# Kernel optimization log

Hardware: AMD Instinct MI355X
Metric: run time of the kernel (lower is better)

The kernel has to match this reference:

```python
import jax, jax.numpy as jnp
import numpy as np

N = 200000      # total nodes
E = 800000      # directed edges
G = 4096        # graphs in batch
D_DRUG = 128
D_CELL = 954
HID = 128
OUT = 128
EPS = 1e-5      # BatchNorm eps


def _bn(x, gamma, beta):
    # training-mode BatchNorm1d (batch statistics, biased var), dropout is eval/identity
    m = jnp.mean(x, axis=0)
    v = jnp.mean((x - m) ** 2, axis=0)
    return gamma * (x - m) * jax.lax.rsqrt(v + EPS) + beta


def _gcn_conv(x, edge_index, W, b):
    # PyG GCNConv: add self-loops, symmetric normalization, aggregate, then bias
    src = jnp.concatenate([edge_index[0], jnp.arange(N)])
    dst = jnp.concatenate([edge_index[1], jnp.arange(N)])
    ones = jnp.ones(src.shape[0], dtype=x.dtype)
    deg = jax.ops.segment_sum(ones, dst, num_segments=N)
    dinv = jnp.where(deg > 0, jax.lax.rsqrt(jnp.maximum(deg, 1.0)), 0.0)
    norm = dinv[src] * dinv[dst]                      # [E+N]
    h = x @ W                                         # [N, out]
    msg = h[src] * norm[:, None]                      # gather + scale
    out = jax.ops.segment_sum(msg, dst, num_segments=N)  # scatter-add
    return out + b


def setup_inputs() -> dict:
    key = jax.random.key(0)
    ks = jax.random.split(key, 12)
    x = jax.random.normal(ks[0], (N, D_DRUG), jnp.float32)
    edge_index = jax.random.randint(ks[1], (2, E), 0, N)
    ibatch = (jnp.arange(N) * G) // N  # sorted, every graph non-empty
    gexpr = jax.random.normal(ks[2], (G, D_CELL), jnp.float32)

    def w(k, shape):
        return jax.random.normal(k, shape, jnp.float32) / np.float32(np.sqrt(shape[0]))

    return {
        "x": x, "edge_index": edge_index, "ibatch": ibatch, "gexpr": gexpr,
        "W1": w(ks[3], (D_DRUG, HID)), "b1": jnp.zeros((HID,), jnp.float32),
        "g1": jnp.ones((HID,), jnp.float32), "be1": jnp.zeros((HID,), jnp.float32),
        "W2": w(ks[4], (HID, OUT)), "b2": jnp.zeros((OUT,), jnp.float32),
        "g2": jnp.ones((OUT,), jnp.float32), "be2": jnp.zeros((OUT,), jnp.float32),
        "Wc1": w(ks[5], (D_CELL, HID)), "bc1": jnp.zeros((HID,), jnp.float32),
        "gc": jnp.ones((HID,), jnp.float32), "bec": jnp.zeros((HID,), jnp.float32),
        "Wc2": w(ks[6], (HID, OUT)), "bc2": jnp.zeros((OUT,), jnp.float32),
    }


def reference(x, edge_index, ibatch, gexpr,
              W1, b1, g1, be1, W2, b2, g2, be2,
              Wc1, bc1, gc, bec, Wc2, bc2):
    # drug branch
    h = _gcn_conv(x, edge_index, W1, b1)
    h = _bn(jax.nn.relu(h), g1, be1)
    h = _gcn_conv(h, edge_index, W2, b2)
    h = _bn(jax.nn.relu(h), g2, be2)
    x_drug = jax.ops.segment_max(h, ibatch, num_segments=G)  # global_max_pool
    # cellline branch
    c = jnp.tanh(gexpr @ Wc1 + bc1)
    c = _bn(c, gc, bec)
    x_cell = jax.nn.relu(c @ Wc2 + bc2)
    return x_drug, x_cell
```

## Files before the change

kernel.cpp:

```cpp
#include <hip/hip_runtime.h>

#define NFEAT 128

typedef __attribute__((ext_vector_type(4))) float f32x4;
typedef __attribute__((ext_vector_type(8))) short bf16x8;

__device__ __forceinline__ unsigned short f2bf(float f) {
    unsigned u = __builtin_bit_cast(unsigned, f);
    u += 0x7fffu + ((u >> 16) & 1u);
    return (unsigned short)(u >> 16);
}
__device__ __forceinline__ float bf2f(unsigned short s) {
    unsigned u = ((unsigned)s) << 16;
    return __builtin_bit_cast(float, u);
}

__device__ __forceinline__ void dma16(const void* g, void* l) {
    __builtin_amdgcn_global_load_lds(
        (const __attribute__((address_space(1))) unsigned int*)g,
        (__attribute__((address_space(3))) unsigned int*)l, 16, 0, 0);
}

template <int ACT, typename OutT, typename AT>
__global__ __launch_bounds__(256) void gemm_dma(
    const AT* __restrict__ A, const unsigned short* __restrict__ Bt,
    OutT* __restrict__ C, int M, int ldA, int ldB,
    const float* __restrict__ bias, const float* __restrict__ dscale)
{
    constexpr bool AF32 = (sizeof(AT) == 4);
    __shared__ AT ash[64 * 128];
    const int tid = threadIdx.x;
    const int wv = tid >> 6, lane = tid & 63;
    const int l16 = lane & 15, quad = lane >> 4;
    const int kbase = blockIdx.y * 128;
    const long tile0 = (long)blockIdx.x * 64;

    const int nc0 = (wv & 1) * 64;
    bf16x8 bfr[4][4];
#pragma unroll
    for (int nt = 0; nt < 4; ++nt) {
        const unsigned short* bp =
            Bt + (size_t)(nc0 + nt * 16 + l16) * ldB + kbase + quad * 8;
#pragma unroll
        for (int ks = 0; ks < 4; ++ks)
            bfr[nt][ks] = *(const bf16x8*)(bp + ks * 32);
    }

    {
        const int r0 = wv * 16;
        if constexpr (AF32) {
#pragma unroll
            for (int j = 0; j < 8; ++j) {
                const float* gp = (const float*)A +
                    (size_t)(tile0 + r0 + j * 2 + (lane >> 5)) * ldA + kbase +
                    (lane & 31) * 4;
                dma16(gp, (void*)&ash[(r0 + j * 2) * 128]);
            }
        } else {
#pragma unroll
            for (int j = 0; j < 4; ++j) {
                const unsigned short* gp = (const unsigned short*)A +
                    (size_t)(tile0 + r0 + j * 4 + (lane >> 4)) * ldA + kbase +
                    l16 * 8;
                dma16(gp, (void*)&ash[(r0 + j * 4) * 128]);
            }
        }
    }
    __syncthreads();

    const int rh = wv >> 1;
    bf16x8 af[2][4];
#pragma unroll
    for (int mt = 0; mt < 2; ++mt) {
        const int row = rh * 32 + mt * 16 + l16;
#pragma unroll
        for (int ks = 0; ks < 4; ++ks) {
            if constexpr (AF32) {
                const float* lp = (const float*)&ash[0] + row * 128 + ks * 32 + quad * 8;
                f32x4 v0 = *(const f32x4*)lp;
                f32x4 v1 = *(const f32x4*)(lp + 4);
                bf16x8 t;
                t[0] = (short)f2bf(v0[0]); t[1] = (short)f2bf(v0[1]);
                t[2] = (short)f2bf(v0[2]); t[3] = (short)f2bf(v0[3]);
                t[4] = (short)f2bf(v1[0]); t[5] = (short)f2bf(v1[1]);
                t[6] = (short)f2bf(v1[2]); t[7] = (short)f2bf(v1[3]);
                af[mt][ks] = t;
            } else {
                af[mt][ks] = *(const bf16x8*)((const unsigned short*)&ash[0] +
                                              row * 128 + ks * 32 + quad * 8);
            }
        }
    }

    f32x4 acc[2][4];
#pragma unroll
    for (int a = 0; a < 2; ++a)
#pragma unroll
        for (int b = 0; b < 4; ++b) acc[a][b] = (f32x4){0.f, 0.f, 0.f, 0.f};
#pragma unroll
    for (int ks = 0; ks < 4; ++ks)
#pragma unroll
        for (int nt = 0; nt < 4; ++nt)
#pragma unroll
            for (int mt = 0; mt < 2; ++mt)
                acc[mt][nt] = __builtin_amdgcn_mfma_f32_16x16x32_bf16(
                    af[mt][ks], bfr[nt][ks], acc[mt][nt], 0, 0, 0);

    C += (size_t)blockIdx.y * M * NFEAT;
    float ds[2][4];
#pragma unroll
    for (int mt = 0; mt < 2; ++mt)
#pragma unroll
        for (int r = 0; r < 4; ++r) {
            long row = tile0 + rh * 32 + mt * 16 + quad * 4 + r;
            ds[mt][r] = dscale ? dscale[row] : 1.f;
        }
#pragma unroll
    for (int nt = 0; nt < 4; ++nt) {
        int col = nc0 + nt * 16 + l16;
        float bv = bias ? bias[col] : 0.f;
#pragma unroll
        for (int mt = 0; mt < 2; ++mt) {
            long rbase = tile0 + rh * 32 + mt * 16 + quad * 4;
#pragma unroll
            for (int r = 0; r < 4; ++r) {
                float v = acc[mt][nt][r] + bv;
                if (ACT == 1) v = tanhf(v);
                if (ACT == 2) v = fmaxf(v, 0.f);
                v *= ds[mt][r];
                if constexpr (sizeof(OutT) == 2)
                    C[(size_t)(rbase + r) * NFEAT + col] = (OutT)f2bf(v);
                else
                    C[(size_t)(rbase + r) * NFEAT + col] = (OutT)v;
            }
        }
    }
}

__global__ void k_transpose(const float* __restrict__ W, unsigned short* __restrict__ Wt,
                            int K, int Kp)
{
    int idx = blockIdx.x * 256 + threadIdx.x;
    if (idx >= 128 * Kp) return;
    int n = idx / Kp, k = idx - n * Kp;
    Wt[idx] = (k < K) ? f2bf(W[(size_t)k * NFEAT + n]) : (unsigned short)0;
}

__global__ void k_bnfold_w(const float* __restrict__ sums8, const float* __restrict__ gamma,
                           const float* __restrict__ beta, float invN,
                           const float* __restrict__ W, const float* __restrict__ extra,
                           unsigned short* __restrict__ Wt, float* __restrict__ brow)
{
    __shared__ float ssc[128], ssh[128];
    int t = threadIdx.x;
    if (t < 128) {
        float s = 0.f, s2 = 0.f;
#pragma unroll
        for (int c = 0; c < 8; ++c) { s += sums8[c * 256 + t]; s2 += sums8[c * 256 + 128 + t]; }
        float mean = s * invN;
        float var = s2 * invN - mean * mean;
        float rstd = rsqrtf(fmaxf(var, 0.f) + 1e-5f);
        float sc = gamma[t] * rstd;
        ssc[t] = sc;
        ssh[t] = beta[t] - mean * sc;
    }
    __syncthreads();
    if (blockIdx.x < 64) {
        int idx = blockIdx.x * 256 + t;
        int n = idx >> 7, k = idx & 127;
        Wt[idx] = f2bf(W[(size_t)k * NFEAT + n] * ssc[k]);
    } else if (t < 128) {
        float s = extra ? extra[t] : 0.f;
        for (int k = 0; k < 128; ++k) s += ssh[k] * W[(size_t)k * NFEAT + t];
        brow[t] = s;
    }
}

__global__ void k_finalize8(const float* __restrict__ sums8, const float* __restrict__ gamma,
                            const float* __restrict__ beta, float* __restrict__ scale,
                            float* __restrict__ shift, float invN)
{
    int j = threadIdx.x;
    float s = 0.f, s2 = 0.f;
#pragma unroll
    for (int c = 0; c < 8; ++c) { s += sums8[c * 256 + j]; s2 += sums8[c * 256 + 128 + j]; }
    float mean = s * invN;
    float var = s2 * invN - mean * mean;
    float rstd = rsqrtf(fmaxf(var, 0.f) + 1e-5f);
    float sc = gamma[j] * rstd;
    scale[j] = sc;
    shift[j] = beta[j] - mean * sc;
}

__global__ void k_padA(const float* __restrict__ g, float* __restrict__ Ap,
                       int G, int DC, int DCP)
{
    long idx = (long)blockIdx.x * 256 + threadIdx.x;
    if (idx >= (long)G * DCP) return;
    long i = idx / DCP; int k = (int)(idx - i * DCP);
    Ap[idx] = (k < DC) ? g[i * DC + k] : 0.f;
}

__global__ void k_degi(const int* __restrict__ dst, int* __restrict__ deg, int E)
{
    int e = blockIdx.x * 256 + threadIdx.x;
    if (e < E) atomicAdd(&deg[dst[e]], 1);
}

__global__ __launch_bounds__(256) void k_scan1(const int* __restrict__ deg,
        int* __restrict__ rowptr, int* __restrict__ bsum, float* __restrict__ dinv, int N)
{
    __shared__ int sh[256];
    int t = threadIdx.x;
    int base = blockIdx.x * 1024 + t * 4;
    int v[4];
#pragma unroll
    for (int j = 0; j < 4; ++j) {
        v[j] = (base + j < N) ? deg[base + j] : 0;
        if (base + j < N) dinv[base + j] = rsqrtf((float)(v[j] + 1));
    }
    int s = v[0] + v[1] + v[2] + v[3];
    sh[t] = s;
    __syncthreads();
    int incl = s;
    for (int off = 1; off < 256; off <<= 1) {
        int x = (t >= off) ? sh[t - off] : 0;
        __syncthreads();
        incl += x;
        sh[t] = incl;
        __syncthreads();
    }
    int run = incl - s;
#pragma unroll
    for (int j = 0; j < 4; ++j) {
        if (base + j < N) rowptr[base + j] = run;
        run += v[j];
    }
    if (t == 255) bsum[blockIdx.x] = incl;
}

__global__ void k_scan2(int* __restrict__ bsum, int nb)
{
    __shared__ int sh[256];
    int t = threadIdx.x;
    int s = (t < nb) ? bsum[t] : 0;
    sh[t] = s;
    __syncthreads();
    int incl = s;
    for (int off = 1; off < 256; off <<= 1) {
        int x = (t >= off) ? sh[t - off] : 0;
        __syncthreads();
        incl += x;
        sh[t] = incl;
        __syncthreads();
    }
    if (t < nb) bsum[t] = incl - s;
}

__global__ void k_scan3(int* __restrict__ rowptr, int* __restrict__ cursor,
                        const int* __restrict__ bsum, int N, int E)
{
    int i = blockIdx.x * 256 + threadIdx.x;
    if (i < N) {
        int v = rowptr[i] + bsum[i >> 10];
        rowptr[i] = v;
        cursor[i] = v;
    } else if (i == N) {
        rowptr[N] = E;
    }
}

__global__ void k_fill(const int* __restrict__ src, const int* __restrict__ dst,
                       int* __restrict__ cursor, int* __restrict__ csr, int E)
{
    int e = blockIdx.x * 256 + threadIdx.x;
    if (e < E) {
        int pos = atomicAdd(&cursor[dst[e]], 1);
        csr[pos] = src[e];
    }
}

__device__ __forceinline__ void unpack_add(float* acc, uint4 a)
{
    acc[0] += bf2f((unsigned short)(a.x & 0xffff));
    acc[1] += bf2f((unsigned short)(a.x >> 16));
    acc[2] += bf2f((unsigned short)(a.y & 0xffff));
    acc[3] += bf2f((unsigned short)(a.y >> 16));
    acc[4] += bf2f((unsigned short)(a.z & 0xffff));
    acc[5] += bf2f((unsigned short)(a.z >> 16));
    acc[6] += bf2f((unsigned short)(a.w & 0xffff));
    acc[7] += bf2f((unsigned short)(a.w >> 16));
}

__device__ __forceinline__ void row_gather(const unsigned short* __restrict__ h,
    const int* __restrict__ rowptr, const int* __restrict__ csr,
    long i, int f, float* acc)
{
    int lo = rowptr[i], hi = rowptr[i + 1];
    int e = lo;
    for (; e + 3 < hi; e += 4) {
        int s0 = csr[e], s1 = csr[e + 1], s2 = csr[e + 2], s3 = csr[e + 3];
        uint4 a = *(const uint4*)(h + ((size_t)s0 << 7) + f);
        uint4 b = *(const uint4*)(h + ((size_t)s1 << 7) + f);
        uint4 c = *(const uint4*)(h + ((size_t)s2 << 7) + f);
        uint4 d = *(const uint4*)(h + ((size_t)s3 << 7) + f);
        unpack_add(acc, a); unpack_add(acc, b);
        unpack_add(acc, c); unpack_add(acc, d);
    }
    for (; e < hi; ++e) {
        int s0 = csr[e];
        uint4 a = *(const uint4*)(h + ((size_t)s0 << 7) + f);
        unpack_add(acc, a);
    }
    uint4 hs = *(const uint4*)(h + ((size_t)i << 7) + f);
    unpack_add(acc, hs);
}

__global__ __launch_bounds__(256) void k_agg(
    const unsigned short* __restrict__ h, const int* __restrict__ rowptr,
    const int* __restrict__ csr, const float* __restrict__ dinv,
    const float* __restrict__ bias, unsigned short* __restrict__ out,
    float* __restrict__ sums8, int N)
{
    __shared__ float red[4][256];
    const int tid = threadIdx.x;
    const int wv = tid >> 6, lane = tid & 63;
    const int f = (tid & 15) << 3;
    const long g0 = (long)blockIdx.x * 16 + (tid >> 4);
    const long gstride = (long)gridDim.x * 16;

    f32x4 b0 = *(const f32x4*)&bias[f];
    f32x4 b1 = *(const f32x4*)&bias[f + 4];

    float s8[8], q8[8];
#pragma unroll
    for (int j = 0; j < 8; ++j) { s8[j] = 0.f; q8[j] = 0.f; }

    for (long i = g0; i < N; i += gstride) {
        float acc[8];
#pragma unroll
        for (int j = 0; j < 8; ++j) acc[j] = 0.f;
        row_gather(h, rowptr, csr, i, f, acc);

        float di = dinv[i];
        unsigned short o[8];
#pragma unroll
        for (int j = 0; j < 8; ++j) {
            float bj = (j < 4) ? b0[j] : b1[j - 4];
            float v = fmaxf(di * acc[j] + bj, 0.f);
            o[j] = f2bf(v);
            s8[j] += v; q8[j] += v * v;
        }
        *(uint4*)(out + (i << 7) + f) = *(const uint4*)o;
    }

#pragma unroll
    for (int j = 0; j < 8; ++j) {
        s8[j] += __shfl_xor(s8[j], 16);
        s8[j] += __shfl_xor(s8[j], 32);
        q8[j] += __shfl_xor(q8[j], 16);
        q8[j] += __shfl_xor(q8[j], 32);
    }
    if (lane < 16) {
#pragma unroll
        for (int j = 0; j < 8; ++j) {
            red[wv][f + j] = s8[j];
            red[wv][128 + f + j] = q8[j];
        }
    }
    __syncthreads();
    float tot = red[0][tid] + red[1][tid] + red[2][tid] + red[3][tid];
    atomicAdd(&sums8[(blockIdx.x & 7) * 256 + tid], tot);
}

__global__ __launch_bounds__(256) void k_aggmax(
    const unsigned short* __restrict__ h, const int* __restrict__ rowptr,
    const int* __restrict__ csr, const float* __restrict__ dinv,
    const float* __restrict__ bias, int* __restrict__ gmax, int* __restrict__ gmin,
    float* __restrict__ sums8, int N, int G)
{
    __shared__ float red[4][256];
    __shared__ int lmax[2][128], lmin[2][128];
    const int tid = threadIdx.x;
    const int wv = tid >> 6, lane = tid & 63;
    const int f = (tid & 15) << 3;
    const int grp = tid >> 4;
    const int g_lo = blockIdx.x * 2;
    const int rstart = (int)(((long long)g_lo * N + G - 1) / G);
    const int rend   = (int)(((long long)(g_lo + 2) * N + G - 1) / G);
    const int bnd1   = (int)(((long long)(g_lo + 1) * N + G - 1) / G);

    for (int idx = tid; idx < 2 * 128; idx += 256) {
        ((int*)lmax)[idx] = 0;
        ((int*)lmin)[idx] = 0x7f800000;
    }
    __syncthreads();

    f32x4 b0 = *(const f32x4*)&bias[f];
    f32x4 b1 = *(const f32x4*)&bias[f + 4];

    float s8[8], q8[8], rmx[8], rmn[8];
#pragma unroll
    for (int j = 0; j < 8; ++j) {
        s8[j] = 0.f; q8[j] = 0.f;
        rmx[j] = 0.f; rmn[j] = __builtin_bit_cast(float, 0x7f800000);
    }
    int cur = 0;

    for (long i = rstart + grp; i < rend; i += 16) {
        float acc[8];
#pragma unroll
        for (int j = 0; j < 8; ++j) acc[j] = 0.f;
        row_gather(h, rowptr, csr, i, f, acc);

        float di = dinv[i];
        int gi = (i >= bnd1);
        if (gi != cur) {
#pragma unroll
            for (int j = 0; j < 8; ++j) {
                atomicMax(&lmax[cur][f + j], __builtin_bit_cast(int, rmx[j]));
                atomicMin(&lmin[cur][f + j], __builtin_bit_cast(int, rmn[j]));
                rmx[j] = 0.f; rmn[j] = __builtin_bit_cast(float, 0x7f800000);
            }
            cur = gi;
        }
#pragma unroll
        for (int j = 0; j < 8; ++j) {
            float bj = (j < 4) ? b0[j] : b1[j - 4];
            float v = fmaxf(di * acc[j] + bj, 0.f);
            s8[j] += v; q8[j] += v * v;
            rmx[j] = fmaxf(rmx[j], v);
            rmn[j] = fminf(rmn[j], v);
        }
    }
#pragma unroll
    for (int j = 0; j < 8; ++j) {
        atomicMax(&lmax[cur][f + j], __builtin_bit_cast(int, rmx[j]));
        atomicMin(&lmin[cur][f + j], __builtin_bit_cast(int, rmn[j]));
    }

#pragma unroll
    for (int j = 0; j < 8; ++j) {
        s8[j] += __shfl_xor(s8[j], 16);
        s8[j] += __shfl_xor(s8[j], 32);
        q8[j] += __shfl_xor(q8[j], 16);
        q8[j] += __shfl_xor(q8[j], 32);
    }
    if (lane < 16) {
#pragma unroll
        for (int j = 0; j < 8; ++j) {
            red[wv][f + j] = s8[j];
            red[wv][128 + f + j] = q8[j];
        }
    }
    __syncthreads();
    float tot = red[0][tid] + red[1][tid] + red[2][tid] + red[3][tid];
    atomicAdd(&sums8[(blockIdx.x & 7) * 256 + tid], tot);

    for (int idx = tid; idx < 2 * 128; idx += 256) {
        int gg = idx >> 7, j = idx & 127;
        gmax[(size_t)(g_lo + gg) * 128 + j] = lmax[gg][j];
        gmin[(size_t)(g_lo + gg) * 128 + j] = lmin[gg][j];
    }
}

__global__ void k_segapply(const int* __restrict__ gmax, const int* __restrict__ gmin,
                           const float* __restrict__ scale, const float* __restrict__ shift,
                           float* __restrict__ out, int total)
{
    int idx = blockIdx.x * 256 + threadIdx.x;
    if (idx >= total) return;
    int j = idx & 127;
    float sc = scale[j], sh = shift[j];
    int bits = (sc >= 0.f) ? gmax[idx] : gmin[idx];
    out[idx] = sc * __builtin_bit_cast(float, bits) + sh;
}

__global__ void k_cellred(const float* __restrict__ p, const float* __restrict__ bias,
                          unsigned short* __restrict__ cbuf, float* __restrict__ sums8, int G)
{
    int j = threadIdx.x & 127;
    int slot = blockIdx.x * 2 + (threadIdx.x >> 7);
    int nslots = gridDim.x * 2;
    const size_t st = (size_t)G * NFEAT;
    float b = bias[j], s = 0.f, s2 = 0.f;
    for (int i = slot; i < G; i += nslots) {
        size_t o = (size_t)i * NFEAT + j;
        float v = b;
#pragma unroll
        for (int c = 0; c < 8; ++c) v += p[o + c * st];
        v = tanhf(v);
        cbuf[o] = f2bf(v);
        s += v; s2 += v * v;
    }
    atomicAdd(&sums8[(blockIdx.x & 7) * 256 + j], s);
    atomicAdd(&sums8[(blockIdx.x & 7) * 256 + 128 + j], s2);
}

extern "C" void kernel_launch(void* const* d_in, const int* in_sizes, int n_in,
                              void* d_out, int out_size, void* d_ws, size_t ws_size,
                              hipStream_t stream)
{
    const float* x     = (const float*)d_in[0];
    const int*   ei    = (const int*)d_in[1];
    const float* gexpr = (const float*)d_in[3];
    const float* W1  = (const float*)d_in[4];
    const float* b1  = (const float*)d_in[5];
    const float* g1  = (const float*)d_in[6];
    const float* be1 = (const float*)d_in[7];
    const float* W2  = (const float*)d_in[8];
    const float* b2  = (const float*)d_in[9];
    const float* g2  = (const float*)d_in[10];
    const float* be2 = (const float*)d_in[11];
    const float* Wc1 = (const float*)d_in[12];
    const float* bc1 = (const float*)d_in[13];
    const float* gc  = (const float*)d_in[14];
    const float* bec = (const float*)d_in[15];
    const float* Wc2 = (const float*)d_in[16];
    const float* bc2 = (const float*)d_in[17];

    const int N = in_sizes[0] / NFEAT;
    const int E = in_sizes[1] / 2;
    const int G = in_sizes[3] / 954;
    const int DC = 954, DCP = 1024;

    char* wsp = (char*)d_ws;
    size_t off = 0;
    auto alloc = [&](size_t bytes) -> char* {
        char* p = wsp + off;
        off += (bytes + 255) & ~(size_t)255;
        return p;
    };
    unsigned short* agg    = (unsigned short*)alloc((size_t)N * NFEAT * 2);
    unsigned short* h      = (unsigned short*)alloc((size_t)N * NFEAT * 2);
    float*          dinv   = (float*)alloc((size_t)N * 4);
    int*            deg    = (int*)alloc((size_t)N * 4);
    int*            rowptr = (int*)alloc((size_t)(N + 1) * 4);
    int*            cursor = (int*)alloc((size_t)N * 4);
    int*            csr    = (int*)alloc((size_t)E * 4);
    int*            bsum   = (int*)alloc(256 * 4);
    float*          Apad   = (float*)alloc((size_t)G * DCP * 4);
    float*          pbuf   = (float*)alloc((size_t)8 * G * NFEAT * 4);
    unsigned short* cbuf   = (unsigned short*)alloc((size_t)G * NFEAT * 2);
    int*            gmax   = (int*)alloc((size_t)G * NFEAT * 4);
    int*            gmin   = (int*)alloc((size_t)G * NFEAT * 4);
    unsigned short* W1t    = (unsigned short*)alloc(128 * 128 * 2);
    unsigned short* W2t    = (unsigned short*)alloc(128 * 128 * 2);
    unsigned short* Wc1t   = (unsigned short*)alloc(128 * DCP * 2);
    unsigned short* Wc2t   = (unsigned short*)alloc(128 * 128 * 2);
    float*          stats  = (float*)alloc(8192 * 4);
    float* sums1 = stats,         * sums2 = stats + 2048, * sumsC = stats + 4096;
    float* scale2 = stats + 6144, * shift2 = stats + 6272;
    float* brow2  = stats + 6400, * browC  = stats + 6528;

    hipMemsetAsync(stats, 0, 6144 * 4, stream);
    hipMemsetAsync(deg, 0, (size_t)N * 4, stream);

    const int* esrc = ei;
    const int* edst = ei + E;

    k_transpose<<<(128 * 128 + 255) / 256, 256, 0, stream>>>(W1, W1t, 128, 128);
    k_transpose<<<(128 * DCP + 255) / 256, 256, 0, stream>>>(Wc1, Wc1t, DC, DCP);
    k_padA<<<(int)(((long)G * DCP + 255) / 256), 256, 0, stream>>>(gexpr, Apad, G, DC, DCP);

    const int nb = (N + 1023) / 1024;
    k_degi<<<(E + 255) / 256, 256, 0, stream>>>(edst, deg, E);
    k_scan1<<<nb, 256, 0, stream>>>(deg, rowptr, bsum, dinv, N);
    k_scan2<<<1, 256, 0, stream>>>(bsum, nb);
    k_scan3<<<(N + 1 + 255) / 256, 256, 0, stream>>>(rowptr, cursor, bsum, N, E);
    k_fill<<<(E + 255) / 256, 256, 0, stream>>>(esrc, edst, cursor, csr, E);

    const int gtiles = N / 64;
    const int ablocks = 2048;

    gemm_dma<0, unsigned short, float><<<dim3(gtiles, 1), 256, 0, stream>>>(
        x, W1t, h, N, 128, 128, nullptr, dinv);
    k_agg<<<ablocks, 256, 0, stream>>>(h, rowptr, csr, dinv, b1, agg, sums1, N);

    k_bnfold_w<<<65, 256, 0, stream>>>(sums1, g1, be1, 1.f / (float)N, W2, nullptr, W2t, brow2);
    gemm_dma<0, unsigned short, unsigned short><<<dim3(gtiles, 1), 256, 0, stream>>>(
        agg, W2t, h, N, 128, 128, brow2, dinv);

    k_aggmax<<<G / 2, 256, 0, stream>>>(h, rowptr, csr, dinv, b2, gmax, gmin, sums2, N, G);
    k_finalize8<<<1, 128, 0, stream>>>(sums2, g2, be2, scale2, shift2, 1.f / (float)N);

    float* outp = (float*)d_out;
    k_segapply<<<(G * NFEAT + 255) / 256, 256, 0, stream>>>(
        gmax, gmin, scale2, shift2, outp, G * NFEAT);

    gemm_dma<0, float, float><<<dim3(G / 64, 8), 256, 0, stream>>>(
        Apad, Wc1t, pbuf, G, DCP, DCP, nullptr, nullptr);
    k_cellred<<<32, 256, 0, stream>>>(pbuf, bc1, cbuf, sumsC, G);
    k_bnfold_w<<<65, 256, 0, stream>>>(sumsC, gc, bec, 1.f / (float)G, Wc2, bc2, Wc2t, browC);
    gemm_dma<2, float, unsigned short><<<dim3(G / 64, 1), 256, 0, stream>>>(
        cbuf, Wc2t, outp + (size_t)G * NFEAT, G, 128, 128, browC, nullptr);
}
```

Before: 515.3 us.

## Merge prep kernels, fuse BN finalize into segapply, pad LDS max/min, nontemporal stores

Merges the weight transposes, the gexpr padding and the degree count into one multi-role launch. Folds the BN-2 finalize into the segment-apply kernel so fewer launches run. Re-indexes the LDS max/min accumulators to a strided, padded layout to cut bank conflicts in the atomics, and writes aggregation output with nontemporal stores. Every segfin block now recomputes the BN statistics, and the hard-coded 512 Wc1t block count assumes DCP equals 1024.

```diff
diff --git a/kernel.cpp b/kernel.cpp
--- a/kernel.cpp
+++ b/kernel.cpp
@@ -4,6 +4,7 @@
 
 typedef __attribute__((ext_vector_type(4))) float f32x4;
 typedef __attribute__((ext_vector_type(8))) short bf16x8;
+typedef __attribute__((ext_vector_type(4))) unsigned int u32x4;
 
 __device__ __forceinline__ unsigned short f2bf(float f) {
     unsigned u = __builtin_bit_cast(unsigned, f);
@@ -137,13 +138,31 @@
     }
 }
 
-__global__ void k_transpose(const float* __restrict__ W, unsigned short* __restrict__ Wt,
-                            int K, int Kp)
-{
-    int idx = blockIdx.x * 256 + threadIdx.x;
-    if (idx >= 128 * Kp) return;
-    int n = idx / Kp, k = idx - n * Kp;
-    Wt[idx] = (k < K) ? f2bf(W[(size_t)k * NFEAT + n]) : (unsigned short)0;
+__global__ void k_prep(const float* __restrict__ W1, unsigned short* __restrict__ W1t,
+                       const float* __restrict__ Wc1, unsigned short* __restrict__ Wc1t,
+                       const float* __restrict__ gexpr, float* __restrict__ Apad,
+                       const int* __restrict__ dst, int* __restrict__ deg,
+                       int G, int DC, int DCP, int E, int r1, int r2, int r3)
+{
+    int b = blockIdx.x, t = threadIdx.x;
+    if (b < r1) {
+        int idx = b * 256 + t;
+        int n = idx >> 7, k = idx & 127;
+        W1t[idx] = f2bf(W1[(size_t)k * NFEAT + n]);
+    } else if (b < r2) {
+        int idx = (b - r1) * 256 + t;
+        int n = idx >> 10, k = idx & 1023;
+        Wc1t[idx] = (k < DC) ? f2bf(Wc1[(size_t)k * NFEAT + n]) : (unsigned short)0;
+    } else if (b < r3) {
+        long idx = (long)(b - r2) * 256 + t;
+        if (idx < (long)G * DCP) {
+            long i = idx / DCP; int k = (int)(idx - i * DCP);
+            Apad[idx] = (k < DC) ? gexpr[i * DC + k] : 0.f;
+        }
+    } else {
+        int e = (b - r3) * 256 + t;
+        if (e < E) atomicAdd(&deg[dst[e]], 1);
+    }
 }
 
 __global__ void k_bnfold_w(const float* __restrict__ sums8, const float* __restrict__ gamma,
@@ -174,37 +193,6 @@
         for (int k = 0; k < 128; ++k) s += ssh[k] * W[(size_t)k * NFEAT + t];
         brow[t] = s;
     }
-}
-
-__global__ void k_finalize8(const float* __restrict__ sums8, const float* __restrict__ gamma,
-                            const float* __restrict__ beta, float* __restrict__ scale,
-                            float* __restrict__ shift, float invN)
-{
-    int j = threadIdx.x;
-    float s = 0.f, s2 = 0.f;
-#pragma unroll
-    for (int c = 0; c < 8; ++c) { s += sums8[c * 256 + j]; s2 += sums8[c * 256 + 128 + j]; }
-    float mean = s * invN;
-    float var = s2 * invN - mean * mean;
-    float rstd = rsqrtf(fmaxf(var, 0.f) + 1e-5f);
-    float sc = gamma[j] * rstd;
-    scale[j] = sc;
-    shift[j] = beta[j] - mean * sc;
-}
-
-__global__ void k_padA(const float* __restrict__ g, float* __restrict__ Ap,
-                       int G, int DC, int DCP)
-{
-    long idx = (long)blockIdx.x * 256 + threadIdx.x;
-    if (idx >= (long)G * DCP) return;
-    long i = idx / DCP; int k = (int)(idx - i * DCP);
-    Ap[idx] = (k < DC) ? g[i * DC + k] : 0.f;
-}
-
-__global__ void k_degi(const int* __restrict__ dst, int* __restrict__ deg, int E)
-{
-    int e = blockIdx.x * 256 + threadIdx.x;
-    if (e < E) atomicAdd(&deg[dst[e]], 1);
 }
 
 __global__ __launch_bounds__(256) void k_scan1(const int* __restrict__ deg,
@@ -351,7 +339,7 @@
             o[j] = f2bf(v);
             s8[j] += v; q8[j] += v * v;
         }
-        *(uint4*)(out + (i << 7) + f) = *(const uint4*)o;
+        __builtin_nontemporal_store(*(const u32x4*)o, (u32x4*)(out + (i << 7) + f));
     }
 
 #pragma unroll
@@ -380,19 +368,20 @@
     float* __restrict__ sums8, int N, int G)
 {
     __shared__ float red[4][256];
-    __shared__ int lmax[2][128], lmin[2][128];
+    __shared__ int lmax[288], lmin[288];
     const int tid = threadIdx.x;
     const int wv = tid >> 6, lane = tid & 63;
-    const int f = (tid & 15) << 3;
+    const int f8 = tid & 15;
+    const int f = f8 << 3;
     const int grp = tid >> 4;
     const int g_lo = blockIdx.x * 2;
     const int rstart = (int)(((long long)g_lo * N + G - 1) / G);
     const int rend   = (int)(((long long)(g_lo + 2) * N + G - 1) / G);
     const int bnd1   = (int)(((long long)(g_lo + 1) * N + G - 1) / G);
 
-    for (int idx = tid; idx < 2 * 128; idx += 256) {
-        ((int*)lmax)[idx] = 0;
-        ((int*)lmin)[idx] = 0x7f800000;
+    for (int idx = tid; idx < 288; idx += 256) {
+        lmax[idx] = 0;
+        lmin[idx] = 0x7f800000;
     }
     __syncthreads();
 
@@ -418,8 +407,8 @@
         if (gi != cur) {
 #pragma unroll
             for (int j = 0; j < 8; ++j) {
-                atomicMax(&lmax[cur][f + j], __builtin_bit_cast(int, rmx[j]));
-                atomicMin(&lmin[cur][f + j], __builtin_bit_cast(int, rmn[j]));
+                atomicMax(&lmax[cur * 144 + j * 16 + f8], __builtin_bit_cast(int, rmx[j]));
+                atomicMin(&lmin[cur * 144 + j * 16 + f8], __builtin_bit_cast(int, rmn[j]));
                 rmx[j] = 0.f; rmn[j] = __builtin_bit_cast(float, 0x7f800000);
             }
             cur = gi;
@@ -435,8 +424,8 @@
     }
 #pragma unroll
     for (int j = 0; j < 8; ++j) {
-        atomicMax(&lmax[cur][f + j], __builtin_bit_cast(int, rmx[j]));
-        atomicMin(&lmin[cur][f + j], __builtin_bit_cast(int, rmn[j]));
+        atomicMax(&lmax[cur * 144 + j * 16 + f8], __builtin_bit_cast(int, rmx[j]));
+        atomicMin(&lmin[cur * 144 + j * 16 + f8], __builtin_bit_cast(int, rmn[j]));
     }
 
 #pragma unroll
@@ -458,22 +447,39 @@
     atomicAdd(&sums8[(blockIdx.x & 7) * 256 + tid], tot);
 
     for (int idx = tid; idx < 2 * 128; idx += 256) {
-        int gg = idx >> 7, j = idx & 127;
-        gmax[(size_t)(g_lo + gg) * 128 + j] = lmax[gg][j];
-        gmin[(size_t)(g_lo + gg) * 128 + j] = lmin[gg][j];
-    }
-}
-
-__global__ void k_segapply(const int* __restrict__ gmax, const int* __restrict__ gmin,
-                           const float* __restrict__ scale, const float* __restrict__ shift,
-                           float* __restrict__ out, int total)
-{
-    int idx = blockIdx.x * 256 + threadIdx.x;
-    if (idx >= total) return;
-    int j = idx & 127;
-    float sc = scale[j], sh = shift[j];
-    int bits = (sc >= 0.f) ? gmax[idx] : gmin[idx];
-    out[idx] = sc * __builtin_bit_cast(float, bits) + sh;
+        int gg = idx >> 7, feat = idx & 127;
+        int a = gg * 144 + (feat & 7) * 16 + (feat >> 3);
+        gmax[(size_t)(g_lo + gg) * 128 + feat] = lmax[a];
+        gmin[(size_t)(g_lo + gg) * 128 + feat] = lmin[a];
+    }
+}
+
+__global__ void k_segfin(const float* __restrict__ sums8, const float* __restrict__ gamma,
+                         const float* __restrict__ beta, const int* __restrict__ gmax,
+                         const int* __restrict__ gmin, float* __restrict__ out,
+                         float invN, int total)
+{
+    __shared__ float ssc[128], ssh[128];
+    int t = threadIdx.x;
+    if (t < 128) {
+        float s = 0.f, s2 = 0.f;
+#pragma unroll
+        for (int c = 0; c < 8; ++c) { s += sums8[c * 256 + t]; s2 += sums8[c * 256 + 128 + t]; }
+        float mean = s * invN;
+        float var = s2 * invN - mean * mean;
+        float rstd = rsqrtf(fmaxf(var, 0.f) + 1e-5f);
+        float sc = gamma[t] * rstd;
+        ssc[t] = sc;
+        ssh[t] = beta[t] - mean * sc;
+    }
+    __syncthreads();
+    int idx = blockIdx.x * 256 + t;
+    if (idx < total) {
+        int j = idx & 127;
+        float sc = ssc[j], sh = ssh[j];
+        int bits = (sc >= 0.f) ? gmax[idx] : gmin[idx];
+        out[idx] = sc * __builtin_bit_cast(float, bits) + sh;
+    }
 }
 
 __global__ void k_cellred(const float* __restrict__ p, const float* __restrict__ bias,
@@ -550,7 +556,6 @@
     unsigned short* Wc2t   = (unsigned short*)alloc(128 * 128 * 2);
     float*          stats  = (float*)alloc(8192 * 4);
     float* sums1 = stats,         * sums2 = stats + 2048, * sumsC = stats + 4096;
-    float* scale2 = stats + 6144, * shift2 = stats + 6272;
     float* brow2  = stats + 6400, * browC  = stats + 6528;
 
     hipMemsetAsync(stats, 0, 6144 * 4, stream);
@@ -559,12 +564,14 @@
     const int* esrc = ei;
     const int* edst = ei + E;
 
-    k_transpose<<<(128 * 128 + 255) / 256, 256, 0, stream>>>(W1, W1t, 128, 128);
-    k_transpose<<<(128 * DCP + 255) / 256, 256, 0, stream>>>(Wc1, Wc1t, DC, DCP);
-    k_padA<<<(int)(((long)G * DCP + 255) / 256), 256, 0, stream>>>(gexpr, Apad, G, DC, DCP);
+    const int r1 = 64;
+    const int r2 = r1 + 512;
+    const int r3 = r2 + (int)(((long)G * DCP + 255) / 256);
+    const int rtot = r3 + (E + 255) / 256;
+    k_prep<<<rtot, 256, 0, stream>>>(W1, W1t, Wc1, Wc1t, gexpr, Apad,
+                                     edst, deg, G, DC, DCP, E, r1, r2, r3);
 
     const int nb = (N + 1023) / 1024;
-    k_degi<<<(E + 255) / 256, 256, 0, stream>>>(edst, deg, E);
     k_scan1<<<nb, 256, 0, stream>>>(deg, rowptr, bsum, dinv, N);
     k_scan2<<<1, 256, 0, stream>>>(bsum, nb);
     k_scan3<<<(N + 1 + 255) / 256, 256, 0, stream>>>(rowptr, cursor, bsum, N, E);
@@ -582,11 +589,10 @@
         agg, W2t, h, N, 128, 128, brow2, dinv);
 
     k_aggmax<<<G / 2, 256, 0, stream>>>(h, rowptr, csr, dinv, b2, gmax, gmin, sums2, N, G);
-    k_finalize8<<<1, 128, 0, stream>>>(sums2, g2, be2, scale2, shift2, 1.f / (float)N);
 
     float* outp = (float*)d_out;
-    k_segapply<<<(G * NFEAT + 255) / 256, 256, 0, stream>>>(
-        gmax, gmin, scale2, shift2, outp, G * NFEAT);
+    k_segfin<<<(G * NFEAT + 255) / 256, 256, 0, stream>>>(
+        sums2, g2, be2, gmax, gmin, outp, 1.f / (float)N, G * NFEAT);
 
     gemm_dma<0, float, float><<<dim3(G / 64, 8), 256, 0, stream>>>(
         Apad, Wc1t, pbuf, G, DCP, DCP, nullptr, nullptr);
```

Measured after the change: 513.2 us. Within noise of the previous version (-0.4%).
